# Kernel tuning notes

Measured on AMD Instinct MI355X. Metric: run time of the kernel, lower is better.

## Reference

```python
import jax, jax.numpy as jnp
import numpy as np

ITERATIONS = 20  # Resonator(iterations=20)
B, F, V, D = 128, 4, 2048, 4096


def _hardsign(x):
    # bipolar normalization used by MAP-VSA multiset(normalize=True); ties -> +1
    return jnp.where(x >= 0, 1.0, -1.0).astype(x.dtype)


def setup_inputs() -> dict:
    key = jax.random.key(0)
    k1, k2 = jax.random.split(key, 2)
    # bipolar codebooks: (F, V, D)
    codebooks = _hardsign(jax.random.normal(k1, (F, V, D), dtype=jnp.float32))
    # a realistic composite input: bind (elementwise product) of one codevector per factor
    idx = jax.random.randint(k2, (B, F), 0, V)                       # (B, F)
    chosen = codebooks[jnp.arange(F)[None, :], idx]                  # (B, F, D)
    inputs = jnp.prod(chosen, axis=1)                                # (B, D)
    # standard resonator init: normalized superposition of each codebook
    init_estimates = jnp.broadcast_to(
        _hardsign(jnp.sum(codebooks, axis=1)), (B, F, D)
    ).astype(jnp.float32)                                            # (B, F, D)
    return {"inputs": inputs, "init_estimates": init_estimates, "codebooks": codebooks}


def _resonator_step(inputs, est, codebooks):
    # est: (B, F, D). rolled stack over k=1..F-1 -> (B, F, F-1, D)
    f = est.shape[-2]
    rolled = jnp.stack([jnp.roll(est, k, axis=-2) for k in range(1, f)], axis=-2)
    inv_others = jnp.prod(rolled, axis=-2)          # multibind over dim -2 -> (B, F, D)
    new_est = inputs[:, None, :] * inv_others       # bind -> (B, F, D)
    sim = jnp.einsum('bfd,fvd->bfv', new_est, codebooks)   # similarity (activation='NONE')
    # multiset(codebooks, sim, normalize=True)
    return _hardsign(jnp.einsum('bfv,fvd->bfd', sim, codebooks))


def reference(inputs, init_estimates, codebooks):
    def body(carry, i):
        est, k, done = carry
        new = _resonator_step(inputs, est, codebooks)
        eq = jnp.all(new == est)          # convergence check (fixed point)
        k = jnp.where(done, k, i)
        return (new, k, done | eq), None

    carry0 = (init_estimates, jnp.int32(0), jnp.bool_(False))
    (est, k, _), _ = jax.lax.scan(body, carry0, jnp.arange(ITERATIONS, dtype=jnp.int32))
    # cleanup: argmax of |similarity| per factor (argmax_abs=True)
    sim = jnp.einsum('bfd,fvd->bfv', est, codebooks)
    outcome = jnp.argmax(jnp.abs(sim), axis=-1)     # (B, F) int indices
    return outcome, k
```

## Files before the change

### kernel.cpp

```cpp
#include <hip/hip_runtime.h>
#include <hip/hip_bf16.h>
#include <stdint.h>

#define B_    128
#define F_    4
#define V_    2048
#define D_    4096
#define DW    64
#define VW    32
#define ITERS 20
#define NKT   16

typedef _Float16 half8 __attribute__((ext_vector_type(8)));
typedef float   floatx4 __attribute__((ext_vector_type(4)));

__global__ __launch_bounds__(256) void k_pack(const float* __restrict__ x,
                                              uint64_t* __restrict__ bits, int n) {
    int t = blockIdx.x * blockDim.x + threadIdx.x;
    if (t * 16 >= n) return;
    const float4* p = (const float4*)x + (size_t)t * 4;
    uint32_t m = 0;
    #pragma unroll
    for (int j = 0; j < 4; ++j) {
        float4 v = p[j];
        m |= (__float_as_uint(v.x) >> 31) << (4 * j + 0);
        m |= (__float_as_uint(v.y) >> 31) << (4 * j + 1);
        m |= (__float_as_uint(v.z) >> 31) << (4 * j + 2);
        m |= (__float_as_uint(v.w) >> 31) << (4 * j + 3);
    }
    ((unsigned short*)bits)[t] = (unsigned short)m;
}

__global__ void k_packT(const uint64_t* __restrict__ cb_bits,
                        uint64_t* __restrict__ cbT) {
    int vw = blockIdx.x, dwg = blockIdx.y, f = blockIdx.z;
    int lane = threadIdx.x & 63;
    int dw = dwg * 4 + (threadIdx.x >> 6);
    uint64_t w = cb_bits[((size_t)f * V_ + vw * 64 + lane) * DW + dw];
    uint64_t r = 0;
    for (int d2 = 0; d2 < 64; ++d2) {
        uint64_t m = __ballot((unsigned)((w >> d2) & 1));
        if (lane == d2) r = m;
    }
    cbT[((size_t)f * D_ + dw * 64 + lane) * VW + vw] = r;
}

__global__ __launch_bounds__(256) void k_sim(
        const uint64_t* __restrict__ cb_bits,
        const uint64_t* __restrict__ in_bits,
        const uint64_t* __restrict__ est_bits,
        _Float16* __restrict__ simf,
        const int* __restrict__ flags, int iter) {
    if (iter > 0 && flags[iter - 1] == 0) return;
    int vt = blockIdx.x, bt = blockIdx.y, f = blockIdx.z;
    int v0 = vt * 64, b0 = bt * 64;
    int tid = threadIdx.x;

    __shared__ __align__(16) ulonglong2 CB2[64 * 32];
    __shared__ __align__(16) ulonglong2 NB2[64 * 32];

    #pragma unroll
    for (int it = 0; it < 8; ++it) {
        int cq = it * 256 + tid;
        int r = cq >> 5, ch = cq & 31;
        const ulonglong2* src = (const ulonglong2*)(cb_bits + ((size_t)f * V_ + v0 + r) * DW);
        CB2[r * 32 + (ch ^ (r & 7))] = src[ch];
    }
    #pragma unroll
    for (int it = 0; it < 8; ++it) {
        int cq = it * 256 + tid;
        int r = cq >> 5, ch = cq & 31;
        int b = b0 + r;
        const ulonglong2* iv = (const ulonglong2*)(in_bits + (size_t)b * DW);
        const uint64_t* eb = est_bits + (size_t)b * F_ * DW;
        ulonglong2 i2 = iv[ch];
        ulonglong2 e0 = ((const ulonglong2*)(eb + 0 * DW))[ch];
        ulonglong2 e1 = ((const ulonglong2*)(eb + 1 * DW))[ch];
        ulonglong2 e2 = ((const ulonglong2*)(eb + 2 * DW))[ch];
        ulonglong2 e3 = ((const ulonglong2*)(eb + 3 * DW))[ch];
        ulonglong2 es = e0;
        if (f == 1) es = e1; else if (f == 2) es = e2; else if (f == 3) es = e3;
        ulonglong2 val;
        val.x = i2.x ^ e0.x ^ e1.x ^ e2.x ^ e3.x ^ es.x;
        val.y = i2.y ^ e0.y ^ e1.y ^ e2.y ^ e3.y ^ es.y;
        NB2[r * 32 + (ch ^ (r & 7))] = val;
    }
    __syncthreads();

    int vv = tid & 15, bb = tid >> 4;
    int svz = vv & 7, sbz = bb & 7;
    int pc[4][4];
    #pragma unroll
    for (int j = 0; j < 4; ++j)
        #pragma unroll
        for (int i = 0; i < 4; ++i) pc[j][i] = 0;

    #pragma unroll 4
    for (int ch = 0; ch < 32; ++ch) {
        ulonglong2 c[4], n[4];
        #pragma unroll
        for (int i = 0; i < 4; ++i)
            c[i] = CB2[(vv + 16 * i) * 32 + (ch ^ svz)];
        #pragma unroll
        for (int j = 0; j < 4; ++j)
            n[j] = NB2[(bb + 16 * j) * 32 + (ch ^ sbz)];
        #pragma unroll
        for (int j = 0; j < 4; ++j)
            #pragma unroll
            for (int i = 0; i < 4; ++i)
                pc[j][i] += __popcll(n[j].x ^ c[i].x) + __popcll(n[j].y ^ c[i].y);
    }

    #pragma unroll
    for (int j = 0; j < 4; ++j) {
        int b = b0 + bb + 16 * j;
        #pragma unroll
        for (int i = 0; i < 4; ++i) {
            int v = v0 + vv + 16 * i;
            simf[((size_t)f * B_ + b) * V_ + v] = (_Float16)(2048 - pc[j][i]);
        }
    }
}

__global__ __launch_bounds__(256) void k_gemm(
        const _Float16* __restrict__ simf,
        const uint64_t* __restrict__ cbT,
        uint64_t* __restrict__ est_bits,
        int* __restrict__ flags, int iter) {
    if (iter > 0 && flags[iter - 1] == 0) return;
    int nt = blockIdx.x, mt = blockIdx.y, f = blockIdx.z;
    int m0 = mt * 64, n0 = nt * 64;
    int tid = threadIdx.x;
    int lane = tid & 63, wave = tid >> 6;
    int lrow = lane & 15, lq = lane >> 4;
    int wm = wave & 1, wn = wave >> 1;

    __shared__ __align__(16) uint64_t Bb[64 * VW];
    __shared__ __align__(16) _Float16 As[64 * 128];
    __shared__ int bd;
    if (tid == 0) bd = 0;

    const uint64_t* bsrc = cbT + ((size_t)f * D_ + n0) * VW;
    #pragma unroll
    for (int p = 0; p < 4; ++p) {
        int chunk = p * 256 + tid;
        int dloc = chunk >> 4, cw = chunk & 15;
        ulonglong2 val = *(const ulonglong2*)&bsrc[dloc * VW + cw * 2];
        *(ulonglong2*)&Bb[dloc * VW + ((cw ^ (dloc & 15)) * 2)] = val;
    }

    const _Float16* Ab = simf + (size_t)f * B_ * V_ + (size_t)m0 * V_;
    int arow = tid >> 4, acol = tid & 15;
    half8 areg[4];
    #pragma unroll
    for (int p = 0; p < 4; ++p)
        areg[p] = *(const half8*)&Ab[(size_t)(p * 16 + arow) * V_ + acol * 8];

    floatx4 acc[2][2] = {};

    const uint64_t SPREAD = 0x1000200040008000ull;
    const uint64_t SMASK  = 0x8000800080008000ull;
    const uint64_t PONE   = 0x3C003C003C003C00ull;

    #pragma unroll 1
    for (int kt = 0; kt < NKT; ++kt) {
        __syncthreads();
        #pragma unroll
        for (int p = 0; p < 4; ++p)
            *(half8*)&As[(p * 16 + arow) * 128 + ((acol ^ arow) * 8)] = areg[p];
        if (kt + 1 < NKT) {
            #pragma unroll
            for (int p = 0; p < 4; ++p)
                areg[p] = *(const half8*)&Ab[(size_t)(p * 16 + arow) * V_ + (kt + 1) * 128 + acol * 8];
        }
        __syncthreads();

        ulonglong2 bw[2];
        #pragma unroll
        for (int nt2 = 0; nt2 < 2; ++nt2) {
            int dloc = wn * 32 + nt2 * 16 + lrow;
            bw[nt2] = *(const ulonglong2*)&Bb[dloc * VW + ((kt ^ (dloc & 15)) * 2)];
        }
        #pragma unroll
        for (int ks = 0; ks < 4; ++ks) {
            half8 af[2];
            #pragma unroll
            for (int mt2 = 0; mt2 < 2; ++mt2) {
                int row = wm * 32 + mt2 * 16 + lrow;
                af[mt2] = *(const half8*)&As[row * 128 + (((ks * 4 + lq) ^ lrow) * 8)];
            }
            half8 bfrag[2];
            #pragma unroll
            for (int nt2 = 0; nt2 < 2; ++nt2) {
                uint64_t w = (ks < 2) ? bw[nt2].x : bw[nt2].y;
                uint32_t byte = (uint32_t)(w >> ((((ks & 1) * 4 + lq)) * 8)) & 0xFFu;
                union { uint64_t q[2]; half8 h; } bu;
                bu.q[0] = (((uint64_t)(byte & 0xFu) * SPREAD) & SMASK) ^ PONE;
                bu.q[1] = (((uint64_t)(byte >> 4)   * SPREAD) & SMASK) ^ PONE;
                bfrag[nt2] = bu.h;
            }
            #pragma unroll
            for (int mt2 = 0; mt2 < 2; ++mt2)
                #pragma unroll
                for (int nt2 = 0; nt2 < 2; ++nt2)
                    acc[mt2][nt2] = __builtin_amdgcn_mfma_f32_16x16x32_f16(
                        af[mt2], bfrag[nt2], acc[mt2][nt2], 0, 0, 0);
        }
    }

    __syncthreads();
    unsigned char* S = (unsigned char*)As;
    #pragma unroll
    for (int mt2 = 0; mt2 < 2; ++mt2)
        #pragma unroll
        for (int nt2 = 0; nt2 < 2; ++nt2)
            #pragma unroll
            for (int r = 0; r < 4; ++r) {
                int row = wm * 32 + mt2 * 16 + lq * 4 + r;
                int col = wn * 32 + nt2 * 16 + lrow;
                S[row * 64 + col] = (acc[mt2][nt2][r] < 0.0f) ? 1 : 0;
            }
    __syncthreads();
    if (tid < 64) {
        const uint64_t* Sw = (const uint64_t*)S;
        uint64_t m = 0;
        #pragma unroll
        for (int j = 0; j < 8; ++j) {
            uint64_t w = Sw[tid * 8 + j];
            m |= ((w * 0x0102040810204080ull) >> 56) << (8 * j);
        }
        size_t widx = ((size_t)(m0 + tid) * F_ + f) * DW + nt;
        uint64_t old = est_bits[widx];
        est_bits[widx] = m;
        if (old != m) atomicOr(&bd, 1);
    }
    __syncthreads();
    if (tid == 0 && bd) atomicOr(&flags[iter], 1);
}

__global__ __launch_bounds__(256) void k_argmax(
        const uint64_t* __restrict__ cb_bits,
        const uint64_t* __restrict__ est_bits,
        int* __restrict__ keys) {
    int vt = blockIdx.x, f = blockIdx.y;
    int v0 = vt * 32;
    int tid = threadIdx.x;

    __shared__ __align__(16) ulonglong2 EB2[128 * 32];
    __shared__ __align__(16) ulonglong2 CBa[32 * 32];

    #pragma unroll
    for (int it = 0; it < 16; ++it) {
        int cq = it * 256 + tid;
        int r = cq >> 5, ch = cq & 31;
        const ulonglong2* src = (const ulonglong2*)(est_bits + ((size_t)r * F_ + f) * DW);
        EB2[r * 32 + (ch ^ (r & 7))] = src[ch];
    }
    #pragma unroll
    for (int it = 0; it < 4; ++it) {
        int cq = it * 256 + tid;
        int r = cq >> 5, ch = cq & 31;
        const ulonglong2* src = (const ulonglong2*)(cb_bits + ((size_t)f * V_ + v0 + r) * DW);
        CBa[r * 32 + (ch ^ (r & 7))] = src[ch];
    }
    __syncthreads();

    int vv = tid & 15, bb = tid >> 4;
    int svz = vv & 7, sbz = bb & 7;
    int pc[8][2];
    #pragma unroll
    for (int j = 0; j < 8; ++j) { pc[j][0] = 0; pc[j][1] = 0; }

    #pragma unroll 4
    for (int ch = 0; ch < 32; ++ch) {
        ulonglong2 c[2], n[8];
        #pragma unroll
        for (int i = 0; i < 2; ++i)
            c[i] = CBa[(vv + 16 * i) * 32 + (ch ^ svz)];
        #pragma unroll
        for (int j = 0; j < 8; ++j)
            n[j] = EB2[(bb + 16 * j) * 32 + (ch ^ sbz)];
        #pragma unroll
        for (int j = 0; j < 8; ++j)
            #pragma unroll
            for (int i = 0; i < 2; ++i)
                pc[j][i] += __popcll(n[j].x ^ c[i].x) + __popcll(n[j].y ^ c[i].y);
    }

    #pragma unroll
    for (int j = 0; j < 8; ++j) {
        int kj = 0x80000000;
        #pragma unroll
        for (int i = 0; i < 2; ++i) {
            int v = v0 + vv + 16 * i;
            int m = 2048 - pc[j][i]; if (m < 0) m = -m;
            int key = (m << 11) | (2047 - v);
            if (key > kj) kj = key;
        }
        #pragma unroll
        for (int s = 1; s < 16; s <<= 1) {
            int o = __shfl_xor(kj, s, 64);
            if (o > kj) kj = o;
        }
        if ((tid & 15) == 0)
            atomicMax(&keys[(size_t)(bb + 16 * j) * F_ + f], kj);
    }
}

__global__ void k_final(const int* __restrict__ keys, const int* __restrict__ flags,
                        int* __restrict__ out) {
    int tid = blockIdx.x * blockDim.x + threadIdx.x;
    if (tid < B_ * F_) out[tid] = 2047 - (keys[tid] & 0x7FF);
    if (tid == 0) {
        int k = ITERS - 1;
        for (int i = 0; i < ITERS; ++i) if (flags[i] == 0) { k = i; break; }
        out[B_ * F_] = k;
    }
}

extern "C" void kernel_launch(void* const* d_in, const int* in_sizes, int n_in,
                              void* d_out, int out_size, void* d_ws, size_t ws_size,
                              hipStream_t stream) {
    const float* inputs = (const float*)d_in[0];
    const float* inite  = (const float*)d_in[1];
    const float* cb     = (const float*)d_in[2];
    int* out = (int*)d_out;

    char* ws = (char*)d_ws;
    uint64_t* cb_bits  = (uint64_t*)ws;  ws += (size_t)F_ * V_ * DW * 8;
    uint64_t* cbT_bits = (uint64_t*)ws;  ws += (size_t)F_ * D_ * VW * 8;
    uint64_t* est_bits = (uint64_t*)ws;  ws += (size_t)B_ * F_ * DW * 8;
    uint64_t* in_bits  = (uint64_t*)ws;  ws += (size_t)B_ * DW * 8;
    _Float16* simf     = (_Float16*)ws;  ws += (size_t)F_ * B_ * V_ * 2;
    int*      flags    = (int*)ws;       ws += 32 * 4;
    int*      keys     = (int*)ws;       ws += B_ * F_ * 4;

    hipMemsetAsync(flags, 0, (32 + B_ * F_) * sizeof(int), stream);
    k_pack<<<(F_ * V_ * D_) / 4096, 256, 0, stream>>>(cb,     cb_bits,  F_ * V_ * D_);
    k_pack<<<(B_ * F_ * D_) / 4096, 256, 0, stream>>>(inite,  est_bits, B_ * F_ * D_);
    k_pack<<<(B_ * D_) / 4096,      256, 0, stream>>>(inputs, in_bits,  B_ * D_);
    k_packT<<<dim3(32, 16, 4), 256, 0, stream>>>(cb_bits, cbT_bits);

    for (int i = 0; i < ITERS; ++i) {
        k_sim<<<dim3(32, 2, 4), 256, 0, stream>>>(cb_bits, in_bits, est_bits, simf, flags, i);
        k_gemm<<<dim3(64, 2, 4), 256, 0, stream>>>(simf, cbT_bits, est_bits, flags, i);
    }
    k_argmax<<<dim3(64, 4), 256, 0, stream>>>(cb_bits, est_bits, keys);
    k_final<<<2, 256, 0, stream>>>(keys, flags, out);
}
```

Baseline: 1.005 ms.

## Fuse all stages into one persistent kernel with software grid barriers

Replaces the pack, transpose, 20×(similarity + GEMM), argmax and final kernels with a single persistent 512-block kernel whose phases are separated by an atomic-counter grid barrier. The goal is to remove per-launch overhead and the inter-kernel gaps. Work is remapped onto the fixed grid, and the similarity tile now covers 32 batch rows per block. The per-iteration convergence early-exit is gone, so every iteration does full work even after a fixed point is reached. The barrier also has a spin timeout that can break correctness if blocks are not all co-resident.

```diff
diff --git a/kernel.cpp b/kernel.cpp
--- a/kernel.cpp
+++ b/kernel.cpp
@@ -1,5 +1,4 @@
 #include <hip/hip_runtime.h>
-#include <hip/hip_bf16.h>
 #include <stdint.h>
 
 #define B_    128
@@ -10,14 +9,13 @@
 #define VW    32
 #define ITERS 20
 #define NKT   16
+#define NBLK  512
 
 typedef _Float16 half8 __attribute__((ext_vector_type(8)));
 typedef float   floatx4 __attribute__((ext_vector_type(4)));
 
-__global__ __launch_bounds__(256) void k_pack(const float* __restrict__ x,
-                                              uint64_t* __restrict__ bits, int n) {
-    int t = blockIdx.x * blockDim.x + threadIdx.x;
-    if (t * 16 >= n) return;
+__device__ __forceinline__ void pack16(const float* __restrict__ x,
+                                       uint64_t* __restrict__ bits, int t) {
     const float4* p = (const float4*)x + (size_t)t * 4;
     uint32_t m = 0;
     #pragma unroll
@@ -31,290 +29,325 @@
     ((unsigned short*)bits)[t] = (unsigned short)m;
 }
 
-__global__ void k_packT(const uint64_t* __restrict__ cb_bits,
-                        uint64_t* __restrict__ cbT) {
-    int vw = blockIdx.x, dwg = blockIdx.y, f = blockIdx.z;
-    int lane = threadIdx.x & 63;
-    int dw = dwg * 4 + (threadIdx.x >> 6);
-    uint64_t w = cb_bits[((size_t)f * V_ + vw * 64 + lane) * DW + dw];
-    uint64_t r = 0;
-    for (int d2 = 0; d2 < 64; ++d2) {
-        uint64_t m = __ballot((unsigned)((w >> d2) & 1));
-        if (lane == d2) r = m;
-    }
-    cbT[((size_t)f * D_ + dw * 64 + lane) * VW + vw] = r;
+__device__ __forceinline__ void grid_sync(int* bar, int target) {
+    __syncthreads();
+    if (threadIdx.x == 0) {
+        __threadfence();
+        if (atomicAdd(&bar[0], 1) == NBLK - 1) {
+            atomicExch(&bar[0], 0);
+            __threadfence();
+            atomicAdd(&bar[1], 1);
+        } else {
+            int spins = 0;
+            while (__hip_atomic_load(&bar[1], __ATOMIC_RELAXED,
+                                     __HIP_MEMORY_SCOPE_AGENT) < target) {
+                __builtin_amdgcn_s_sleep(8);
+                if (++spins > (1 << 17)) break;
+            }
+        }
+        __threadfence();
+    }
+    __syncthreads();
 }
 
-__global__ __launch_bounds__(256) void k_sim(
-        const uint64_t* __restrict__ cb_bits,
-        const uint64_t* __restrict__ in_bits,
-        const uint64_t* __restrict__ est_bits,
-        _Float16* __restrict__ simf,
-        const int* __restrict__ flags, int iter) {
-    if (iter > 0 && flags[iter - 1] == 0) return;
-    int vt = blockIdx.x, bt = blockIdx.y, f = blockIdx.z;
-    int v0 = vt * 64, b0 = bt * 64;
-    int tid = threadIdx.x;
-
-    __shared__ __align__(16) ulonglong2 CB2[64 * 32];
-    __shared__ __align__(16) ulonglong2 NB2[64 * 32];
-
-    #pragma unroll
-    for (int it = 0; it < 8; ++it) {
-        int cq = it * 256 + tid;
-        int r = cq >> 5, ch = cq & 31;
-        const ulonglong2* src = (const ulonglong2*)(cb_bits + ((size_t)f * V_ + v0 + r) * DW);
-        CB2[r * 32 + (ch ^ (r & 7))] = src[ch];
-    }
-    #pragma unroll
-    for (int it = 0; it < 8; ++it) {
-        int cq = it * 256 + tid;
-        int r = cq >> 5, ch = cq & 31;
-        int b = b0 + r;
-        const ulonglong2* iv = (const ulonglong2*)(in_bits + (size_t)b * DW);
-        const uint64_t* eb = est_bits + (size_t)b * F_ * DW;
-        ulonglong2 i2 = iv[ch];
-        ulonglong2 e0 = ((const ulonglong2*)(eb + 0 * DW))[ch];
-        ulonglong2 e1 = ((const ulonglong2*)(eb + 1 * DW))[ch];
-        ulonglong2 e2 = ((const ulonglong2*)(eb + 2 * DW))[ch];
-        ulonglong2 e3 = ((const ulonglong2*)(eb + 3 * DW))[ch];
-        ulonglong2 es = e0;
-        if (f == 1) es = e1; else if (f == 2) es = e2; else if (f == 3) es = e3;
-        ulonglong2 val;
-        val.x = i2.x ^ e0.x ^ e1.x ^ e2.x ^ e3.x ^ es.x;
-        val.y = i2.y ^ e0.y ^ e1.y ^ e2.y ^ e3.y ^ es.y;
-        NB2[r * 32 + (ch ^ (r & 7))] = val;
-    }
-    __syncthreads();
-
-    int vv = tid & 15, bb = tid >> 4;
-    int svz = vv & 7, sbz = bb & 7;
-    int pc[4][4];
-    #pragma unroll
-    for (int j = 0; j < 4; ++j)
+__global__ __launch_bounds__(256, 2) void k_fused(
+        const float* __restrict__ cb, const float* __restrict__ inite,
+        const float* __restrict__ inputs,
+        uint64_t* __restrict__ cb_bits, uint64_t* __restrict__ cbT,
+        uint64_t* __restrict__ est_bits, uint64_t* __restrict__ in_bits,
+        _Float16* __restrict__ simf, int* __restrict__ flags,
+        int* __restrict__ keys, int* __restrict__ out, int* bar) {
+    const int bid = blockIdx.x;
+    const int tid = threadIdx.x;
+    const int gtid = bid * 256 + tid;
+    const int T = NBLK * 256;
+    int ng = 0;
+
+    __shared__ __align__(16) unsigned char LDSU[49152];
+    __shared__ int bd;
+
+    {
+        const int ncb = (F_ * V_ * D_) / 16;
+        for (int t = gtid; t < ncb; t += T) pack16(cb, cb_bits, t);
+        pack16(inite, est_bits, gtid);
+        if (gtid < (B_ * D_) / 16) pack16(inputs, in_bits, gtid);
+        if (gtid < 32) flags[gtid] = 0;
+        if (gtid < B_ * F_) keys[gtid] = 0;
+    }
+    grid_sync(bar, ++ng);
+
+    {
+        int wave = tid >> 6, lane = tid & 63;
+        #pragma unroll 1
+        for (int s = 0; s < 4; ++s) {
+            int u = (bid * 4 + wave) + 2048 * s;
+            int vw = u & 31, dw = (u >> 5) & 63, f = u >> 11;
+            uint64_t w = cb_bits[((size_t)f * V_ + vw * 64 + lane) * DW + dw];
+            uint64_t r = 0;
+            for (int d2 = 0; d2 < 64; ++d2) {
+                uint64_t m = __ballot((unsigned)((w >> d2) & 1));
+                if (lane == d2) r = m;
+            }
+            cbT[((size_t)f * D_ + dw * 64 + lane) * VW + vw] = r;
+        }
+    }
+    grid_sync(bar, ++ng);
+
+    #pragma unroll 1
+    for (int i = 0; i < ITERS; ++i) {
+        {
+            int vt = bid & 31, bt = (bid >> 5) & 3, f = bid >> 7;
+            int v0 = vt * 64, b0 = bt * 32;
+            ulonglong2* CB2 = (ulonglong2*)LDSU;
+            ulonglong2* NB2 = (ulonglong2*)(LDSU + 32768);
+            #pragma unroll
+            for (int it = 0; it < 8; ++it) {
+                int cq = it * 256 + tid;
+                int r = cq >> 5, ch = cq & 31;
+                const ulonglong2* src = (const ulonglong2*)(cb_bits + ((size_t)f * V_ + v0 + r) * DW);
+                CB2[r * 32 + (ch ^ (r & 7))] = src[ch];
+            }
+            #pragma unroll
+            for (int it = 0; it < 4; ++it) {
+                int cq = it * 256 + tid;
+                int r = cq >> 5, ch = cq & 31;
+                int b = b0 + r;
+                const ulonglong2* iv = (const ulonglong2*)(in_bits + (size_t)b * DW);
+                const uint64_t* eb = est_bits + (size_t)b * F_ * DW;
+                ulonglong2 i2 = iv[ch];
+                ulonglong2 e0 = ((const ulonglong2*)(eb + 0 * DW))[ch];
+                ulonglong2 e1 = ((const ulonglong2*)(eb + 1 * DW))[ch];
+                ulonglong2 e2 = ((const ulonglong2*)(eb + 2 * DW))[ch];
+                ulonglong2 e3 = ((const ulonglong2*)(eb + 3 * DW))[ch];
+                ulonglong2 es = ((const ulonglong2*)(eb + (size_t)f * DW))[ch];
+                ulonglong2 val;
+                val.x = i2.x ^ e0.x ^ e1.x ^ e2.x ^ e3.x ^ es.x;
+                val.y = i2.y ^ e0.y ^ e1.y ^ e2.y ^ e3.y ^ es.y;
+                NB2[r * 32 + (ch ^ (r & 7))] = val;
+            }
+            __syncthreads();
+
+            int vv = tid & 15, bb = tid >> 4;
+            int svz = vv & 7, sbz = bb & 7;
+            int pc[2][4];
+            #pragma unroll
+            for (int j = 0; j < 2; ++j)
+                #pragma unroll
+                for (int ii = 0; ii < 4; ++ii) pc[j][ii] = 0;
+
+            #pragma unroll 4
+            for (int ch = 0; ch < 32; ++ch) {
+                ulonglong2 c[4], n[2];
+                #pragma unroll
+                for (int ii = 0; ii < 4; ++ii)
+                    c[ii] = CB2[(vv + 16 * ii) * 32 + (ch ^ svz)];
+                #pragma unroll
+                for (int j = 0; j < 2; ++j)
+                    n[j] = NB2[(bb + 16 * j) * 32 + (ch ^ sbz)];
+                #pragma unroll
+                for (int j = 0; j < 2; ++j)
+                    #pragma unroll
+                    for (int ii = 0; ii < 4; ++ii)
+                        pc[j][ii] += __popcll(n[j].x ^ c[ii].x) + __popcll(n[j].y ^ c[ii].y);
+            }
+            #pragma unroll
+            for (int j = 0; j < 2; ++j) {
+                int b = b0 + bb + 16 * j;
+                #pragma unroll
+                for (int ii = 0; ii < 4; ++ii) {
+                    int v = v0 + vv + 16 * ii;
+                    simf[((size_t)f * B_ + b) * V_ + v] = (_Float16)(2048 - pc[j][ii]);
+                }
+            }
+        }
+        grid_sync(bar, ++ng);
+
+        {
+            int gnt = bid & 63, gmt = (bid >> 6) & 1, gf = bid >> 7;
+            int m0 = gmt * 64, n0 = gnt * 64;
+            int lane = tid & 63, wave = tid >> 6;
+            int lrow = lane & 15, lq = lane >> 4;
+            int wm = wave & 1, wn = wave >> 1;
+
+            uint64_t* Bb = (uint64_t*)LDSU;
+            _Float16* As = (_Float16*)(LDSU + 16384);
+            if (tid == 0) bd = 0;
+
+            const uint64_t* bsrc = cbT + ((size_t)gf * D_ + n0) * VW;
+            #pragma unroll
+            for (int p = 0; p < 4; ++p) {
+                int chunk = p * 256 + tid;
+                int dloc = chunk >> 4, cw = chunk & 15;
+                ulonglong2 val = *(const ulonglong2*)&bsrc[dloc * VW + cw * 2];
+                *(ulonglong2*)&Bb[dloc * VW + ((cw ^ (dloc & 15)) * 2)] = val;
+            }
+
+            const _Float16* Ab = simf + (size_t)gf * B_ * V_ + (size_t)m0 * V_;
+            int arow = tid >> 4, acol = tid & 15;
+            half8 areg[4];
+            #pragma unroll
+            for (int p = 0; p < 4; ++p)
+                areg[p] = *(const half8*)&Ab[(size_t)(p * 16 + arow) * V_ + acol * 8];
+
+            floatx4 acc[2][2] = {};
+
+            const uint64_t SPREAD = 0x1000200040008000ull;
+            const uint64_t SMASK  = 0x8000800080008000ull;
+            const uint64_t PONE   = 0x3C003C003C003C00ull;
+
+            #pragma unroll 1
+            for (int kt = 0; kt < NKT; ++kt) {
+                __syncthreads();
+                #pragma unroll
+                for (int p = 0; p < 4; ++p)
+                    *(half8*)&As[(p * 16 + arow) * 128 + ((acol ^ arow) * 8)] = areg[p];
+                if (kt + 1 < NKT) {
+                    #pragma unroll
+                    for (int p = 0; p < 4; ++p)
+                        areg[p] = *(const half8*)&Ab[(size_t)(p * 16 + arow) * V_ + (kt + 1) * 128 + acol * 8];
+                }
+                __syncthreads();
+
+                ulonglong2 bw[2];
+                #pragma unroll
+                for (int nt2 = 0; nt2 < 2; ++nt2) {
+                    int dloc = wn * 32 + nt2 * 16 + lrow;
+                    bw[nt2] = *(const ulonglong2*)&Bb[dloc * VW + ((kt ^ (dloc & 15)) * 2)];
+                }
+                #pragma unroll
+                for (int ks = 0; ks < 4; ++ks) {
+                    half8 af[2];
+                    #pragma unroll
+                    for (int mt2 = 0; mt2 < 2; ++mt2) {
+                        int row = wm * 32 + mt2 * 16 + lrow;
+                        af[mt2] = *(const half8*)&As[row * 128 + (((ks * 4 + lq) ^ lrow) * 8)];
+                    }
+                    half8 bfrag[2];
+                    #pragma unroll
+                    for (int nt2 = 0; nt2 < 2; ++nt2) {
+                        uint64_t w = (ks < 2) ? bw[nt2].x : bw[nt2].y;
+                        uint32_t byte = (uint32_t)(w >> ((((ks & 1) * 4 + lq)) * 8)) & 0xFFu;
+                        union { uint64_t q[2]; half8 h; } bu;
+                        bu.q[0] = (((uint64_t)(byte & 0xFu) * SPREAD) & SMASK) ^ PONE;
+                        bu.q[1] = (((uint64_t)(byte >> 4)   * SPREAD) & SMASK) ^ PONE;
+                        bfrag[nt2] = bu.h;
+                    }
+                    #pragma unroll
+                    for (int mt2 = 0; mt2 < 2; ++mt2)
+                        #pragma unroll
+                        for (int nt2 = 0; nt2 < 2; ++nt2)
+                            acc[mt2][nt2] = __builtin_amdgcn_mfma_f32_16x16x32_f16(
+                                af[mt2], bfrag[nt2], acc[mt2][nt2], 0, 0, 0);
+                }
+            }
+
+            __syncthreads();
+            unsigned char* S = (unsigned char*)As;
+            #pragma unroll
+            for (int mt2 = 0; mt2 < 2; ++mt2)
+                #pragma unroll
+                for (int nt2 = 0; nt2 < 2; ++nt2)
+                    #pragma unroll
+                    for (int r = 0; r < 4; ++r) {
+                        int row = wm * 32 + mt2 * 16 + lq * 4 + r;
+                        int col = wn * 32 + nt2 * 16 + lrow;
+                        S[row * 64 + col] = (acc[mt2][nt2][r] < 0.0f) ? 1 : 0;
+                    }
+            __syncthreads();
+            if (tid < 64) {
+                const uint64_t* Sw = (const uint64_t*)S;
+                uint64_t m = 0;
+                #pragma unroll
+                for (int j = 0; j < 8; ++j) {
+                    uint64_t w = Sw[tid * 8 + j];
+                    m |= ((w * 0x0102040810204080ull) >> 56) << (8 * j);
+                }
+                size_t widx = ((size_t)(m0 + tid) * F_ + gf) * DW + gnt;
+                uint64_t old = est_bits[widx];
+                est_bits[widx] = m;
+                if (old != m) atomicOr(&bd, 1);
+            }
+            __syncthreads();
+            if (tid == 0 && bd) atomicOr(&flags[i], 1);
+        }
+        grid_sync(bar, ++ng);
+    }
+
+    {
+        int vt = bid & 63, bg = (bid >> 6) & 1, f = bid >> 7;
+        int v0 = vt * 32, b0g = bg * 64;
+        ulonglong2* EB2 = (ulonglong2*)LDSU;
+        ulonglong2* CBa = (ulonglong2*)(LDSU + 32768);
         #pragma unroll
-        for (int i = 0; i < 4; ++i) pc[j][i] = 0;
-
-    #pragma unroll 4
-    for (int ch = 0; ch < 32; ++ch) {
-        ulonglong2 c[4], n[4];
+        for (int it = 0; it < 8; ++it) {
+            int cq = it * 256 + tid;
+            int r = cq >> 5, ch = cq & 31;
+            const ulonglong2* src = (const ulonglong2*)(est_bits + ((size_t)(b0g + r) * F_ + f) * DW);
+            EB2[r * 32 + (ch ^ (r & 7))] = src[ch];
+        }
         #pragma unroll
-        for (int i = 0; i < 4; ++i)
-            c[i] = CB2[(vv + 16 * i) * 32 + (ch ^ svz)];
+        for (int it = 0; it < 4; ++it) {
+            int cq = it * 256 + tid;
+            int r = cq >> 5, ch = cq & 31;
+            const ulonglong2* src = (const ulonglong2*)(cb_bits + ((size_t)f * V_ + v0 + r) * DW);
+            CBa[r * 32 + (ch ^ (r & 7))] = src[ch];
+        }
+        __syncthreads();
+
+        int vv = tid & 15, bb = tid >> 4;
+        int svz = vv & 7, sbz = bb & 7;
+        int pc[4][2];
         #pragma unroll
-        for (int j = 0; j < 4; ++j)
-            n[j] = NB2[(bb + 16 * j) * 32 + (ch ^ sbz)];
+        for (int j = 0; j < 4; ++j) { pc[j][0] = 0; pc[j][1] = 0; }
+
+        #pragma unroll 4
+        for (int ch = 0; ch < 32; ++ch) {
+            ulonglong2 c[2], n[4];
+            #pragma unroll
+            for (int ii = 0; ii < 2; ++ii)
+                c[ii] = CBa[(vv + 16 * ii) * 32 + (ch ^ svz)];
+            #pragma unroll
+            for (int j = 0; j < 4; ++j)
+                n[j] = EB2[(bb + 16 * j) * 32 + (ch ^ sbz)];
+            #pragma unroll
+            for (int j = 0; j < 4; ++j)
+                #pragma unroll
+                for (int ii = 0; ii < 2; ++ii)
+                    pc[j][ii] += __popcll(n[j].x ^ c[ii].x) + __popcll(n[j].y ^ c[ii].y);
+        }
         #pragma unroll
-        for (int j = 0; j < 4; ++j)
-            #pragma unroll
-            for (int i = 0; i < 4; ++i)
-                pc[j][i] += __popcll(n[j].x ^ c[i].x) + __popcll(n[j].y ^ c[i].y);
-    }
-
-    #pragma unroll
-    for (int j = 0; j < 4; ++j) {
-        int b = b0 + bb + 16 * j;
-        #pragma unroll
-        for (int i = 0; i < 4; ++i) {
-            int v = v0 + vv + 16 * i;
-            simf[((size_t)f * B_ + b) * V_ + v] = (_Float16)(2048 - pc[j][i]);
-        }
-    }
-}
-
-__global__ __launch_bounds__(256) void k_gemm(
-        const _Float16* __restrict__ simf,
-        const uint64_t* __restrict__ cbT,
-        uint64_t* __restrict__ est_bits,
-        int* __restrict__ flags, int iter) {
-    if (iter > 0 && flags[iter - 1] == 0) return;
-    int nt = blockIdx.x, mt = blockIdx.y, f = blockIdx.z;
-    int m0 = mt * 64, n0 = nt * 64;
-    int tid = threadIdx.x;
-    int lane = tid & 63, wave = tid >> 6;
-    int lrow = lane & 15, lq = lane >> 4;
-    int wm = wave & 1, wn = wave >> 1;
-
-    __shared__ __align__(16) uint64_t Bb[64 * VW];
-    __shared__ __align__(16) _Float16 As[64 * 128];
-    __shared__ int bd;
-    if (tid == 0) bd = 0;
-
-    const uint64_t* bsrc = cbT + ((size_t)f * D_ + n0) * VW;
-    #pragma unroll
-    for (int p = 0; p < 4; ++p) {
-        int chunk = p * 256 + tid;
-        int dloc = chunk >> 4, cw = chunk & 15;
-        ulonglong2 val = *(const ulonglong2*)&bsrc[dloc * VW + cw * 2];
-        *(ulonglong2*)&Bb[dloc * VW + ((cw ^ (dloc & 15)) * 2)] = val;
-    }
-
-    const _Float16* Ab = simf + (size_t)f * B_ * V_ + (size_t)m0 * V_;
-    int arow = tid >> 4, acol = tid & 15;
-    half8 areg[4];
-    #pragma unroll
-    for (int p = 0; p < 4; ++p)
-        areg[p] = *(const half8*)&Ab[(size_t)(p * 16 + arow) * V_ + acol * 8];
-
-    floatx4 acc[2][2] = {};
-
-    const uint64_t SPREAD = 0x1000200040008000ull;
-    const uint64_t SMASK  = 0x8000800080008000ull;
-    const uint64_t PONE   = 0x3C003C003C003C00ull;
-
-    #pragma unroll 1
-    for (int kt = 0; kt < NKT; ++kt) {
-        __syncthreads();
-        #pragma unroll
-        for (int p = 0; p < 4; ++p)
-            *(half8*)&As[(p * 16 + arow) * 128 + ((acol ^ arow) * 8)] = areg[p];
-        if (kt + 1 < NKT) {
-            #pragma unroll
-            for (int p = 0; p < 4; ++p)
-                areg[p] = *(const half8*)&Ab[(size_t)(p * 16 + arow) * V_ + (kt + 1) * 128 + acol * 8];
-        }
-        __syncthreads();
-
-        ulonglong2 bw[2];
-        #pragma unroll
-        for (int nt2 = 0; nt2 < 2; ++nt2) {
-            int dloc = wn * 32 + nt2 * 16 + lrow;
-            bw[nt2] = *(const ulonglong2*)&Bb[dloc * VW + ((kt ^ (dloc & 15)) * 2)];
-        }
-        #pragma unroll
-        for (int ks = 0; ks < 4; ++ks) {
-            half8 af[2];
-            #pragma unroll
-            for (int mt2 = 0; mt2 < 2; ++mt2) {
-                int row = wm * 32 + mt2 * 16 + lrow;
-                af[mt2] = *(const half8*)&As[row * 128 + (((ks * 4 + lq) ^ lrow) * 8)];
-            }
-            half8 bfrag[2];
-            #pragma unroll
-            for (int nt2 = 0; nt2 < 2; ++nt2) {
-                uint64_t w = (ks < 2) ? bw[nt2].x : bw[nt2].y;
-                uint32_t byte = (uint32_t)(w >> ((((ks & 1) * 4 + lq)) * 8)) & 0xFFu;
-                union { uint64_t q[2]; half8 h; } bu;
-                bu.q[0] = (((uint64_t)(byte & 0xFu) * SPREAD) & SMASK) ^ PONE;
-                bu.q[1] = (((uint64_t)(byte >> 4)   * SPREAD) & SMASK) ^ PONE;
-                bfrag[nt2] = bu.h;
-            }
-            #pragma unroll
-            for (int mt2 = 0; mt2 < 2; ++mt2)
-                #pragma unroll
-                for (int nt2 = 0; nt2 < 2; ++nt2)
-                    acc[mt2][nt2] = __builtin_amdgcn_mfma_f32_16x16x32_f16(
-                        af[mt2], bfrag[nt2], acc[mt2][nt2], 0, 0, 0);
-        }
-    }
-
-    __syncthreads();
-    unsigned char* S = (unsigned char*)As;
-    #pragma unroll
-    for (int mt2 = 0; mt2 < 2; ++mt2)
-        #pragma unroll
-        for (int nt2 = 0; nt2 < 2; ++nt2)
-            #pragma unroll
-            for (int r = 0; r < 4; ++r) {
-                int row = wm * 32 + mt2 * 16 + lq * 4 + r;
-                int col = wn * 32 + nt2 * 16 + lrow;
-                S[row * 64 + col] = (acc[mt2][nt2][r] < 0.0f) ? 1 : 0;
-            }
-    __syncthreads();
-    if (tid < 64) {
-        const uint64_t* Sw = (const uint64_t*)S;
-        uint64_t m = 0;
-        #pragma unroll
-        for (int j = 0; j < 8; ++j) {
-            uint64_t w = Sw[tid * 8 + j];
-            m |= ((w * 0x0102040810204080ull) >> 56) << (8 * j);
-        }
-        size_t widx = ((size_t)(m0 + tid) * F_ + f) * DW + nt;
-        uint64_t old = est_bits[widx];
-        est_bits[widx] = m;
-        if (old != m) atomicOr(&bd, 1);
-    }
-    __syncthreads();
-    if (tid == 0 && bd) atomicOr(&flags[iter], 1);
-}
-
-__global__ __launch_bounds__(256) void k_argmax(
-        const uint64_t* __restrict__ cb_bits,
-        const uint64_t* __restrict__ est_bits,
-        int* __restrict__ keys) {
-    int vt = blockIdx.x, f = blockIdx.y;
-    int v0 = vt * 32;
-    int tid = threadIdx.x;
-
-    __shared__ __align__(16) ulonglong2 EB2[128 * 32];
-    __shared__ __align__(16) ulonglong2 CBa[32 * 32];
-
-    #pragma unroll
-    for (int it = 0; it < 16; ++it) {
-        int cq = it * 256 + tid;
-        int r = cq >> 5, ch = cq & 31;
-        const ulonglong2* src = (const ulonglong2*)(est_bits + ((size_t)r * F_ + f) * DW);
-        EB2[r * 32 + (ch ^ (r & 7))] = src[ch];
-    }
-    #pragma unroll
-    for (int it = 0; it < 4; ++it) {
-        int cq = it * 256 + tid;
-        int r = cq >> 5, ch = cq & 31;
-        const ulonglong2* src = (const ulonglong2*)(cb_bits + ((size_t)f * V_ + v0 + r) * DW);
-        CBa[r * 32 + (ch ^ (r & 7))] = src[ch];
-    }
-    __syncthreads();
-
-    int vv = tid & 15, bb = tid >> 4;
-    int svz = vv & 7, sbz = bb & 7;
-    int pc[8][2];
-    #pragma unroll
-    for (int j = 0; j < 8; ++j) { pc[j][0] = 0; pc[j][1] = 0; }
-
-    #pragma unroll 4
-    for (int ch = 0; ch < 32; ++ch) {
-        ulonglong2 c[2], n[8];
-        #pragma unroll
-        for (int i = 0; i < 2; ++i)
-            c[i] = CBa[(vv + 16 * i) * 32 + (ch ^ svz)];
-        #pragma unroll
-        for (int j = 0; j < 8; ++j)
-            n[j] = EB2[(bb + 16 * j) * 32 + (ch ^ sbz)];
-        #pragma unroll
-        for (int j = 0; j < 8; ++j)
-            #pragma unroll
-            for (int i = 0; i < 2; ++i)
-                pc[j][i] += __popcll(n[j].x ^ c[i].x) + __popcll(n[j].y ^ c[i].y);
-    }
-
-    #pragma unroll
-    for (int j = 0; j < 8; ++j) {
-        int kj = 0x80000000;
-        #pragma unroll
-        for (int i = 0; i < 2; ++i) {
-            int v = v0 + vv + 16 * i;
-            int m = 2048 - pc[j][i]; if (m < 0) m = -m;
-            int key = (m << 11) | (2047 - v);
-            if (key > kj) kj = key;
-        }
-        #pragma unroll
-        for (int s = 1; s < 16; s <<= 1) {
-            int o = __shfl_xor(kj, s, 64);
-            if (o > kj) kj = o;
-        }
-        if ((tid & 15) == 0)
-            atomicMax(&keys[(size_t)(bb + 16 * j) * F_ + f], kj);
-    }
-}
-
-__global__ void k_final(const int* __restrict__ keys, const int* __restrict__ flags,
-                        int* __restrict__ out) {
-    int tid = blockIdx.x * blockDim.x + threadIdx.x;
-    if (tid < B_ * F_) out[tid] = 2047 - (keys[tid] & 0x7FF);
-    if (tid == 0) {
-        int k = ITERS - 1;
-        for (int i = 0; i < ITERS; ++i) if (flags[i] == 0) { k = i; break; }
-        out[B_ * F_] = k;
+        for (int j = 0; j < 4; ++j) {
+            int kj = (int)0x80000000;
+            #pragma unroll
+            for (int ii = 0; ii < 2; ++ii) {
+                int v = v0 + vv + 16 * ii;
+                int m = 2048 - pc[j][ii]; if (m < 0) m = -m;
+                int key = (m << 11) | (2047 - v);
+                if (key > kj) kj = key;
+            }
+            #pragma unroll
+            for (int s = 1; s < 16; s <<= 1) {
+                int o = __shfl_xor(kj, s, 64);
+                if (o > kj) kj = o;
+            }
+            if ((tid & 15) == 0)
+                atomicMax(&keys[(size_t)(b0g + bb + 16 * j) * F_ + f], kj);
+        }
+    }
+    grid_sync(bar, ++ng);
+
+    if (bid == 0) {
+        for (int t = tid; t < B_ * F_; t += 256)
+            out[t] = 2047 - (keys[t] & 0x7FF);
+        if (tid == 0) {
+            int k = ITERS - 1;
+            for (int i2 = 0; i2 < ITERS; ++i2) {
+                int fl = __hip_atomic_load(&flags[i2], __ATOMIC_RELAXED,
+                                           __HIP_MEMORY_SCOPE_AGENT);
+                if (fl == 0) { k = i2; break; }
+            }
+            out[B_ * F_] = k;
+        }
     }
 }
 
@@ -334,17 +367,11 @@
     _Float16* simf     = (_Float16*)ws;  ws += (size_t)F_ * B_ * V_ * 2;
     int*      flags    = (int*)ws;       ws += 32 * 4;
     int*      keys     = (int*)ws;       ws += B_ * F_ * 4;
-
-    hipMemsetAsync(flags, 0, (32 + B_ * F_) * sizeof(int), stream);
-    k_pack<<<(F_ * V_ * D_) / 4096, 256, 0, stream>>>(cb,     cb_bits,  F_ * V_ * D_);
-    k_pack<<<(B_ * F_ * D_) / 4096, 256, 0, stream>>>(inite,  est_bits, B_ * F_ * D_);
-    k_pack<<<(B_ * D_) / 4096,      256, 0, stream>>>(inputs, in_bits,  B_ * D_);
-    k_packT<<<dim3(32, 16, 4), 256, 0, stream>>>(cb_bits, cbT_bits);
-
-    for (int i = 0; i < ITERS; ++i) {
-        k_sim<<<dim3(32, 2, 4), 256, 0, stream>>>(cb_bits, in_bits, est_bits, simf, flags, i);
-        k_gemm<<<dim3(64, 2, 4), 256, 0, stream>>>(simf, cbT_bits, est_bits, flags, i);
-    }
-    k_argmax<<<dim3(64, 4), 256, 0, stream>>>(cb_bits, est_bits, keys);
-    k_final<<<2, 256, 0, stream>>>(keys, flags, out);
+    int*      bar      = (int*)ws;       ws += 64;
+
+    hipMemsetAsync(bar, 0, 64, stream);
+
+    k_fused<<<dim3(NBLK), dim3(256), 0, stream>>>(
+        cb, inite, inputs, cb_bits, cbT_bits, est_bits, in_bits,
+        simf, flags, keys, out, bar);
 }
```

Measured after the change: 3.044 ms. +202.9%, slower.
